# Performance work log

Hardware: AMD Instinct MI355X
Metric: run time of the kernel (lower is better)

The kernel has to match this reference:

```python
import jax, jax.numpy as jnp
import numpy as np
import math

B, L, D, H = 2, 1024, 1024, 16
DK = D // H  # 64
R = 130      # 2k+2 relative-position buckets (k=64)


def setup_inputs() -> dict:
    key = jax.random.key(0)
    ks = jax.random.split(key, 16)
    s = 1.0 / math.sqrt(D)
    return {
        "hidden_state": jax.random.normal(ks[0], (B, L, D), jnp.float32),
        "rel_q": jax.random.normal(ks[1], (1, H, R, DK), jnp.float32),
        "rel_k": jax.random.normal(ks[2], (1, H, R, DK), jnp.float32),
        "Wq": jax.random.normal(ks[3], (D, D), jnp.float32) * s,
        "bq": jnp.zeros((D,), jnp.float32),
        "Wk": jax.random.normal(ks[4], (D, D), jnp.float32) * s,
        "bk": jnp.zeros((D,), jnp.float32),
        "Wv": jax.random.normal(ks[5], (D, D), jnp.float32) * s,
        "bv": jnp.zeros((D,), jnp.float32),
        "Wo": jax.random.normal(ks[6], (D, D), jnp.float32) * s,
        "bo": jnp.zeros((D,), jnp.float32),
        "pos_indices": jax.random.randint(ks[7], (B, H, L, L), 0, R, jnp.int64 if jax.config.jax_enable_x64 else jnp.int32),
        "mask": jax.random.bernoulli(ks[8], 0.1, (B, 1, 1, L)),
    }


def reference(hidden_state, rel_q, rel_k, Wq, bq, Wk, bk, Wv, bv, Wo, bo, pos_indices, mask):
    # projections (torch Linear: x @ W.T + b), split into heads -> [B,H,L,DK]
    def proj(x, W, b):
        return (x @ W.T + b).reshape(B, L, H, DK).transpose(0, 2, 1, 3)

    q = proj(hidden_state, Wq, bq)
    k = proj(hidden_state, Wk, bk)
    v = proj(hidden_state, Wv, bv)

    scale = 1.0 / math.sqrt(DK * 3)  # scale_factor = 3 (c2c + p2c + c2p)

    # content-to-content: [B,H,L,L]
    c2c = jnp.einsum("bhid,bhjd->bhij", q, k) * scale

    # position-to-content: rel_q @ k.T -> [B,H,R,L], gather rows by pos_indices
    p2c = jnp.einsum("hrd,bhjd->bhrj", rel_q[0] * scale, k)
    p2c = jnp.take_along_axis(p2c, pos_indices, axis=-2)  # [B,H,L,L]

    # content-to-position: q @ rel_k.T -> [B,H,L,R], gather cols by pos_indices.T
    c2p = jnp.einsum("bhid,hrd->bhir", q, rel_k[0]) * scale
    c2p = jnp.take_along_axis(c2p, jnp.swapaxes(pos_indices, -2, -1), axis=-1)  # [B,H,L,L]

    scores = c2c + p2c + c2p
    scores = jnp.where(mask, jnp.float32(-1e9), scores)
    probs = jax.nn.softmax(scores, axis=-1)  # dropout p=0.0 (eval)

    ctx = jnp.einsum("bhij,bhjd->bhid", probs, v)
    out = ctx.transpose(0, 2, 1, 3).reshape(B, L, D) @ Wo.T + bo
    return out
```

## Files before the change

### kernel.cpp

```cpp
#include <hip/hip_runtime.h>
#include <hip/hip_fp16.h>

typedef _Float16 f16;
typedef f16 f16x8 __attribute__((ext_vector_type(8)));
typedef f16 f16x4 __attribute__((ext_vector_type(4)));
typedef float f32x4 __attribute__((ext_vector_type(4)));

#define DEVI static __device__ __forceinline__

constexpr int Bc = 2, Lc = 1024, Dc = 1024, Hc = 16, DKc = 64, Rc = 130;
constexpr float SCALE = 0.07216878364870323f;
constexpr float MASKV = -30000.0f;

DEVI uint2 pack8(int4 a, int4 b) {
    unsigned lo = (unsigned)(a.x & 255) | ((unsigned)(a.y & 255) << 8) |
                  ((unsigned)(a.z & 255) << 16) | ((unsigned)(a.w & 255) << 24);
    unsigned hi = (unsigned)(b.x & 255) | ((unsigned)(b.y & 255) << 8) |
                  ((unsigned)(b.z & 255) << 16) | ((unsigned)(b.w & 255) << 24);
    return make_uint2(lo, hi);
}

DEVI int i4get(const int4& v, int u) {
    return u == 0 ? v.x : (u == 1 ? v.y : (u == 2 ? v.z : v.w));
}

__global__ __launch_bounds__(256) void gemm_qkv(const float* __restrict__ A,
                                                const float* __restrict__ wq,
                                                const float* __restrict__ wk,
                                                const float* __restrict__ wv,
                                                const float* __restrict__ bq,
                                                const float* __restrict__ bk,
                                                const float* __restrict__ bv,
                                                f16* __restrict__ qw,
                                                f16* __restrict__ kw,
                                                f16* __restrict__ vtw) {
    constexpr int K = 1024;
    __shared__ __align__(16) f16 As[128][40];
    __shared__ __align__(16) f16 Bs[64][40];
    const int tid = threadIdx.x, lane = tid & 63, w = tid >> 6;
    const int wm = w >> 1, wn = w & 1;
    const int m0 = blockIdx.y * 128, n0 = blockIdx.x * 64;
    const int which = n0 >> 10;
    const float* __restrict__ W = which == 0 ? wq : (which == 1 ? wk : wv);
    const int n0L = n0 & 1023;

    f32x4 acc[4][2];
#pragma unroll
    for (int i = 0; i < 4; ++i)
#pragma unroll
        for (int j = 0; j < 2; ++j) acc[i][j] = (f32x4){0.f, 0.f, 0.f, 0.f};

    for (int k0 = 0; k0 < K; k0 += 32) {
#pragma unroll
        for (int rep = 0; rep < 4; ++rep) {
            int id = tid + rep * 256;
            int row = id >> 3, c = (id & 7) * 4;
            float4 v = *(const float4*)&A[(size_t)(m0 + row) * K + k0 + c];
            *(f16x4*)&As[row][c] = (f16x4){(f16)v.x, (f16)v.y, (f16)v.z, (f16)v.w};
        }
#pragma unroll
        for (int rep = 0; rep < 2; ++rep) {
            int id = tid + rep * 256;
            int row = id >> 3, c = (id & 7) * 4;
            float4 v = *(const float4*)&W[(size_t)(n0L + row) * K + k0 + c];
            *(f16x4*)&Bs[row][c] = (f16x4){(f16)v.x, (f16)v.y, (f16)v.z, (f16)v.w};
        }
        __syncthreads();
        f16x8 a[4], bb[2];
#pragma unroll
        for (int mf = 0; mf < 4; ++mf)
            a[mf] = *(const f16x8*)&As[wm * 64 + mf * 16 + (lane & 15)][(lane >> 4) * 8];
#pragma unroll
        for (int nf = 0; nf < 2; ++nf)
            bb[nf] = *(const f16x8*)&Bs[wn * 32 + nf * 16 + (lane & 15)][(lane >> 4) * 8];
#pragma unroll
        for (int mf = 0; mf < 4; ++mf)
#pragma unroll
            for (int nf = 0; nf < 2; ++nf)
                acc[mf][nf] = __builtin_amdgcn_mfma_f32_16x16x32_f16(a[mf], bb[nf], acc[mf][nf], 0, 0, 0);
        __syncthreads();
    }

    const float* bp = which == 0 ? bq : (which == 1 ? bk : bv);
    const float scl = which == 0 ? SCALE : 1.0f;
#pragma unroll
    for (int mf = 0; mf < 4; ++mf)
#pragma unroll
        for (int nf = 0; nf < 2; ++nf) {
            int rowb = m0 + wm * 64 + mf * 16 + (lane >> 4) * 4;
            int col = n0 + wn * 32 + nf * 16 + (lane & 15);
            int colL = col & 1023;
            int h = colL >> 6, d = colL & 63;
            float bv_ = bp[colL];
            if (which == 2) {
                int b = rowb >> 10, i = rowb & (Lc - 1);
                f16x4 pk = {(f16)(acc[mf][nf][0] + bv_), (f16)(acc[mf][nf][1] + bv_),
                            (f16)(acc[mf][nf][2] + bv_), (f16)(acc[mf][nf][3] + bv_)};
                *(f16x4*)&vtw[(((size_t)(b * Hc + h)) * DKc + d) * Lc + i] = pk;
            } else {
                f16* dst = which ? kw : qw;
#pragma unroll
                for (int rg = 0; rg < 4; ++rg) {
                    int row = rowb + rg;
                    int b = row >> 10, i = row & (Lc - 1);
                    dst[(((size_t)(b * Hc + h)) * Lc + i) * DKc + d] =
                        (f16)((acc[mf][nf][rg] + bv_) * scl);
                }
            }
        }
}

__global__ __launch_bounds__(256) void rel_mfma(const f16* __restrict__ rowmat,
                                                const float* __restrict__ relmat,
                                                f16* __restrict__ outT, float scl) {
    __shared__ __align__(16) f16 As[144][72];
    __shared__ __align__(16) f16 Bs[64][72];
    const int tid = threadIdx.x, lane = tid & 63, w = tid >> 6;
    const int bh = blockIdx.y, h = bh & (Hc - 1);
    const int i0 = blockIdx.x * 64;
    const size_t bhR = (size_t)bh * Rc;

    for (int e = tid; e < Rc * 16; e += 256) {
        int r = e >> 4, c = (e & 15) * 4;
        float4 v = *(const float4*)&relmat[((size_t)h * Rc + r) * DKc + c];
        *(f16x4*)&As[r][c] = (f16x4){(f16)v.x, (f16)v.y, (f16)v.z, (f16)v.w};
    }
    if (tid < 224) {
        int r = 130 + (tid >> 4), c = (tid & 15) * 4;
        *(f16x4*)&As[r][c] = (f16x4){(f16)0.f, (f16)0.f, (f16)0.f, (f16)0.f};
    }
    for (int e = tid; e < 64 * 8; e += 256) {
        int i = e >> 3, c = (e & 7) * 8;
        *(f16x8*)&Bs[i][c] = *(const f16x8*)&rowmat[((size_t)bh * Lc + i0 + i) * DKc + c];
    }
    __syncthreads();

    f16x8 bfr[2];
#pragma unroll
    for (int ks = 0; ks < 2; ++ks)
        bfr[ks] = *(const f16x8*)&Bs[w * 16 + (lane & 15)][ks * 32 + (lane >> 4) * 8];
    f32x4 acc[9];
#pragma unroll
    for (int m = 0; m < 9; ++m) acc[m] = (f32x4){0.f, 0.f, 0.f, 0.f};
#pragma unroll
    for (int m = 0; m < 9; ++m)
#pragma unroll
        for (int ks = 0; ks < 2; ++ks) {
            f16x8 af = *(const f16x8*)&As[m * 16 + (lane & 15)][ks * 32 + (lane >> 4) * 8];
            acc[m] = __builtin_amdgcn_mfma_f32_16x16x32_f16(af, bfr[ks], acc[m], 0, 0, 0);
        }
#pragma unroll
    for (int m = 0; m < 9; ++m)
#pragma unroll
        for (int rg = 0; rg < 4; ++rg) {
            int r = m * 16 + (lane >> 4) * 4 + rg;
            if (r < Rc)
                outT[(bhR + r) * Lc + i0 + w * 16 + (lane & 15)] = (f16)(acc[m][rg] * scl);
        }
}

__global__ __launch_bounds__(512) void attn_v8(const f16* __restrict__ q,
                                               const f16* __restrict__ k,
                                               const f16* __restrict__ vt,
                                               const f16* __restrict__ p2c,
                                               const f16* __restrict__ c2pT,
                                               const int* __restrict__ pos,
                                               const int* __restrict__ mask,
                                               f16* __restrict__ opart,
                                               float2* __restrict__ mlpart) {
    __shared__ f16 tc2p[Rc][132];
    __shared__ f16 tp2c[2][Rc][36];
    __shared__ __align__(16) f16 Ks[2][32][72];
    __shared__ unsigned char pJI[2][32][136];
    __shared__ float madd[2][32];
    __shared__ __align__(16) f16 Pl[8][16][32];

    const int tid = threadIdx.x, lane = tid & 63, w = tid >> 6;
    const int flat = blockIdx.x;
    const int ib = flat >> 6;
    const int sp = (flat >> 5) & 1;
    const int bh = flat & 31;
    const int b = bh >> 4, h = bh & 15;
    const int i0 = ib * 128;
    const int j0base = sp * 512;
    const size_t bhL = (size_t)bh * Lc;
    const size_t bhR = (size_t)bh * Rc;
    f16* __restrict__ op = opart + (size_t)sp * Bc * Lc * Dc;
    float2* __restrict__ mlp = mlpart + (size_t)sp * Bc * Hc * Lc;
    const int g = lane >> 4, il16 = lane & 15, irow = w * 16 + il16;

    for (int e = tid; e < Rc * 32; e += 512) {
        int r = e >> 5, c4 = (e & 31) * 4;
        *(f16x4*)&tc2p[r][c4] = *(const f16x4*)&c2pT[(bhR + r) * Lc + i0 + c4];
    }

    f16x8 qa[2];
    {
        const f16* qp = &q[(bhL + i0 + irow) * DKc + g * 8];
        qa[0] = *(const f16x8*)qp;
        qa[1] = *(const f16x8*)(qp + 32);
    }

    float mrun = -1e30f, lrun = 0.f;
    f32x4 oacc[4];
#pragma unroll
    for (int df = 0; df < 4; ++df) oacc[df] = (f32x4){0.f, 0.f, 0.f, 0.f};

    f16x4 kreg;
    int4 prA0, prA1, prB0, prB1;
    f16x4 tpr0, tpr1, tpr2;
    uint2 pjreg;
    float mreg;

#define FV_ISSUE(J0X)                                                                        \
    {                                                                                        \
        kreg = *(const f16x4*)&k[(bhL + (J0X) + (tid >> 4)) * DKc + (tid & 15) * 4];         \
        {                                                                                    \
            int e_ = tid;                                                                    \
            tpr0 = *(const f16x4*)&p2c[(bhR + (e_ >> 3)) * Lc + (J0X) + (e_ & 7) * 4];       \
            e_ = tid + 512;                                                                  \
            tpr1 = *(const f16x4*)&p2c[(bhR + (e_ >> 3)) * Lc + (J0X) + (e_ & 7) * 4];       \
            if (tid < 16) {                                                                  \
                e_ = tid + 1024;                                                             \
                tpr2 = *(const f16x4*)&p2c[(bhR + (e_ >> 3)) * Lc + (J0X) + (e_ & 7) * 4];   \
            }                                                                                \
        }                                                                                    \
        {                                                                                    \
            const int* pp = &pos[(bhL + (J0X) + (tid >> 4)) * Lc + i0 + (tid & 15) * 8];     \
            pjreg = pack8(*(const int4*)pp, *(const int4*)(pp + 4));                         \
        }                                                                                    \
        if (tid < 32) mreg = mask[b * Lc + (J0X) + tid] ? MASKV : 0.f;                       \
        {                                                                                    \
            const int* prow = &pos[(bhL + i0 + irow) * Lc + (J0X) + g * 4];                  \
            prB0 = *(const int4*)prow;                                                       \
            prB1 = *(const int4*)(prow + 16);                                                \
        }                                                                                    \
    }

#define FV_COMMIT(NB)                                                                        \
    {                                                                                        \
        *(f16x4*)&Ks[NB][tid >> 4][(tid & 15) * 4] = kreg;                                   \
        int e_ = tid;                                                                        \
        *(f16x4*)&tp2c[NB][e_ >> 3][(e_ & 7) * 4] = tpr0;                                    \
        e_ = tid + 512;                                                                      \
        *(f16x4*)&tp2c[NB][e_ >> 3][(e_ & 7) * 4] = tpr1;                                    \
        if (tid < 16) { e_ = tid + 1024; *(f16x4*)&tp2c[NB][e_ >> 3][(e_ & 7) * 4] = tpr2; } \
        *(uint2*)&pJI[NB][tid >> 4][(tid & 15) * 8] = pjreg;                                 \
        if (tid < 32) madd[NB][tid] = mreg;                                                  \
    }

    FV_ISSUE(j0base);
    FV_COMMIT(0);
    prA0 = prB0; prA1 = prB1;
    __syncthreads();

    for (int t = 0; t < 16; ++t) {
        const int cur = t & 1;
        const int j0 = j0base + t * 32;
        if (t < 15) FV_ISSUE(j0 + 32);

        f32x4 s[2];
        s[0] = (f32x4){0.f, 0.f, 0.f, 0.f};
        s[1] = (f32x4){0.f, 0.f, 0.f, 0.f};
#pragma unroll
        for (int jf = 0; jf < 2; ++jf)
#pragma unroll
            for (int ks = 0; ks < 2; ++ks) {
                f16x8 kb = *(const f16x8*)&Ks[cur][jf * 16 + il16][ks * 32 + g * 8];
                s[jf] = __builtin_amdgcn_mfma_f32_16x16x32_f16(kb, qa[ks], s[jf], 0, 0, 0);
            }

        f16x8 vf[4];
#pragma unroll
        for (int df = 0; df < 4; ++df)
            vf[df] = *(const f16x8*)&vt[((size_t)bh * DKc + df * 16 + il16) * Lc + j0 + g * 8];

        float sv[8];
#pragma unroll
        for (int u = 0; u < 8; ++u) {
            int jcol = (u < 4) ? (g * 4 + u) : (16 + g * 4 + (u - 4));
            int r1 = (u < 4) ? i4get(prA0, u) : i4get(prA1, u - 4);
            int r2 = pJI[cur][jcol][irow];
            sv[u] = s[u >> 2][u & 3] + (float)tp2c[cur][r1][jcol] +
                    (float)tc2p[r2][irow] + madd[cur][jcol];
        }

        float tm = sv[0];
#pragma unroll
        for (int e = 1; e < 8; ++e) tm = fmaxf(tm, sv[e]);
        tm = fmaxf(tm, __shfl_xor(tm, 16));
        tm = fmaxf(tm, __shfl_xor(tm, 32));
        float mnew = fmaxf(mrun, tm);
        float alpha = __expf(mrun - mnew);
        float rs = 0.f;
#pragma unroll
        for (int e = 0; e < 8; ++e) {
            sv[e] = __expf(sv[e] - mnew);
            rs += sv[e];
        }
        rs += __shfl_xor(rs, 16);
        rs += __shfl_xor(rs, 32);
        lrun = lrun * alpha + rs;
        mrun = mnew;

#pragma unroll
        for (int jf = 0; jf < 2; ++jf) {
            f16x4 pk = {(f16)sv[jf * 4 + 0], (f16)sv[jf * 4 + 1],
                        (f16)sv[jf * 4 + 2], (f16)sv[jf * 4 + 3]};
            *(f16x4*)&Pl[w][il16][jf * 16 + g * 4] = pk;
        }

        float al[4];
#pragma unroll
        for (int rg = 0; rg < 4; ++rg)
            al[rg] = __shfl(alpha, (lane & 48) | (g * 4 + rg));
#pragma unroll
        for (int df = 0; df < 4; ++df)
#pragma unroll
            for (int rg = 0; rg < 4; ++rg) oacc[df][rg] *= al[rg];

        f16x8 pa = *(const f16x8*)&Pl[w][il16][g * 8];
#pragma unroll
        for (int df = 0; df < 4; ++df)
            oacc[df] = __builtin_amdgcn_mfma_f32_16x16x32_f16(pa, vf[df], oacc[df], 0, 0, 0);

        if (t < 15) {
            FV_COMMIT(cur ^ 1);
            prA0 = prB0; prA1 = prB1;
        }
        __syncthreads();
    }

#pragma unroll
    for (int df = 0; df < 4; ++df)
#pragma unroll
        for (int rg = 0; rg < 4; ++rg) {
            int i = i0 + w * 16 + g * 4 + rg;
            int d = df * 16 + il16;
            op[((size_t)(b * Lc + i) * Hc + h) * DKc + d] = (f16)oacc[df][rg];
        }
    if (g == 0) mlp[bhL + i0 + irow] = make_float2(mrun, lrun);
#undef FV_ISSUE
#undef FV_COMMIT
}

__global__ __launch_bounds__(256) void merge_ns(const f16* __restrict__ op,
                                                const float2* __restrict__ ml,
                                                f16* __restrict__ ctx, int ns) {
    int t4 = blockIdx.x * 256 + threadIdx.x;
    int t = t4 * 4;
    int b = t >> 20;
    int rem = t & 1048575;
    int i = rem >> 10;
    int h = (rem & 1023) >> 6;
    int row = ((b << 4) + h) * Lc + i;
    const size_t On = (size_t)Bc * Lc * Dc, Mn = (size_t)Bc * Hc * Lc;
    float mx = -1e30f;
    for (int s = 0; s < ns; ++s) mx = fmaxf(mx, ml[s * Mn + row].x);
    float l = 0.f;
    float v[4] = {0.f, 0.f, 0.f, 0.f};
    for (int s = 0; s < ns; ++s) {
        float2 m = ml[s * Mn + row];
        float w_ = __expf(m.x - mx);
        l += m.y * w_;
        f16x4 o = *(const f16x4*)&op[s * On + t];
#pragma unroll
        for (int e = 0; e < 4; ++e) v[e] += (float)o[e] * w_;
    }
    float rl = 1.0f / l;
    f16x4 r = {(f16)(v[0] * rl), (f16)(v[1] * rl), (f16)(v[2] * rl), (f16)(v[3] * rl)};
    *(f16x4*)&ctx[t] = r;
}

__global__ __launch_bounds__(256) void gemm_out(const f16* __restrict__ A,
                                                const float* __restrict__ W,
                                                const float* __restrict__ bias,
                                                float* __restrict__ outf) {
    constexpr int K = 1024;
    __shared__ __align__(16) f16 As[128][40];
    __shared__ __align__(16) f16 Bs[64][40];
    const int tid = threadIdx.x, lane = tid & 63, w = tid >> 6;
    const int wm = w >> 1, wn = w & 1;
    const int m0 = blockIdx.y * 128, n0 = blockIdx.x * 64;

    f32x4 acc[4][2];
#pragma unroll
    for (int i = 0; i < 4; ++i)
#pragma unroll
        for (int j = 0; j < 2; ++j) acc[i][j] = (f32x4){0.f, 0.f, 0.f, 0.f};

    for (int k0 = 0; k0 < K; k0 += 32) {
#pragma unroll
        for (int rep = 0; rep < 2; ++rep) {
            int id = tid + rep * 256;
            int row = id >> 2, c = (id & 3) * 8;
            *(f16x8*)&As[row][c] = *(const f16x8*)&A[(size_t)(m0 + row) * K + k0 + c];
        }
#pragma unroll
        for (int rep = 0; rep < 2; ++rep) {
            int id = tid + rep * 256;
            int row = id >> 3, c = (id & 7) * 4;
            float4 v = *(const float4*)&W[(size_t)(n0 + row) * K + k0 + c];
            *(f16x4*)&Bs[row][c] = (f16x4){(f16)v.x, (f16)v.y, (f16)v.z, (f16)v.w};
        }
        __syncthreads();
        f16x8 a[4], bb[2];
#pragma unroll
        for (int mf = 0; mf < 4; ++mf)
            a[mf] = *(const f16x8*)&As[wm * 64 + mf * 16 + (lane & 15)][(lane >> 4) * 8];
#pragma unroll
        for (int nf = 0; nf < 2; ++nf)
            bb[nf] = *(const f16x8*)&Bs[wn * 32 + nf * 16 + (lane & 15)][(lane >> 4) * 8];
#pragma unroll
        for (int mf = 0; mf < 4; ++mf)
#pragma unroll
            for (int nf = 0; nf < 2; ++nf)
                acc[mf][nf] = __builtin_amdgcn_mfma_f32_16x16x32_f16(a[mf], bb[nf], acc[mf][nf], 0, 0, 0);
        __syncthreads();
    }
#pragma unroll
    for (int mf = 0; mf < 4; ++mf)
#pragma unroll
        for (int nf = 0; nf < 2; ++nf) {
            int rowb = m0 + wm * 64 + mf * 16 + (lane >> 4) * 4;
            int col = n0 + wn * 32 + nf * 16 + (lane & 15);
            float bv = bias[col];
#pragma unroll
            for (int rg = 0; rg < 4; ++rg)
                outf[(size_t)(rowb + rg) * Dc + col] = acc[mf][nf][rg] + bv;
        }
}

extern "C" void kernel_launch(void* const* d_in, const int* in_sizes, int n_in,
                              void* d_out, int out_size, void* d_ws, size_t ws_size,
                              hipStream_t stream) {
    const float* hid = (const float*)d_in[0];
    const float* rel_q = (const float*)d_in[1];
    const float* rel_k = (const float*)d_in[2];
    const float* Wq = (const float*)d_in[3];
    const float* bq = (const float*)d_in[4];
    const float* Wk = (const float*)d_in[5];
    const float* bk = (const float*)d_in[6];
    const float* Wv = (const float*)d_in[7];
    const float* bv = (const float*)d_in[8];
    const float* Wo = (const float*)d_in[9];
    const float* bo = (const float*)d_in[10];
    const int* pos = (const int*)d_in[11];
    const int* mask = (const int*)d_in[12];

    const size_t MiB = 1ull << 20;
    const size_t tblBytes = (size_t)Bc * Hc * Rc * Lc * 2;
    const size_t opBytes = (size_t)Bc * Lc * Dc * 2;
    const size_t mlBytes = (size_t)Bc * Hc * Lc * 8;
    const size_t need = (12 + 18 + 13) * MiB + 65536;
    if (need > ws_size) return;

    char* ws = (char*)d_ws;
    size_t off = 0;
    auto alloc = [&](size_t bytes) {
        void* p = ws + off;
        off += (bytes + 255) & ~(size_t)255;
        return p;
    };

    f16* qw = (f16*)alloc(opBytes);
    f16* kw = (f16*)alloc(opBytes);
    f16* vtw = (f16*)alloc(opBytes);
    f16* c2pTw = (f16*)alloc(tblBytes);
    f16* p2cw = (f16*)alloc(tblBytes);
    char* u = (char*)alloc(13 * MiB);
    f16* oparts = (f16*)u;
    float2* mls = (float2*)(u + 2 * opBytes);
    f16* ctxh = (f16*)(u + 2 * (opBytes + mlBytes));

    gemm_qkv<<<dim3(48, 16), 256, 0, stream>>>(hid, Wq, Wk, Wv, bq, bk, bv, qw, kw, vtw);
    rel_mfma<<<dim3(16, 32), 256, 0, stream>>>(qw, rel_k, c2pTw, 1.0f);
    rel_mfma<<<dim3(16, 32), 256, 0, stream>>>(kw, rel_q, p2cw, SCALE);
    attn_v8<<<512, 512, 0, stream>>>(qw, kw, vtw, p2cw, c2pTw, pos, mask, oparts, mls);
    merge_ns<<<2048, 256, 0, stream>>>(oparts, mls, ctxh, 2);
    gemm_out<<<dim3(16, 16), 256, 0, stream>>>(ctxh, Wo, bo, (float*)d_out);
}
```

Before: 150.1 us.

## Stage V tiles in shared memory and pass P via lane shuffles

The attention kernel now loads each V^T tile once per block into a double-buffered shared-memory buffer through the existing prefetch/commit pipeline, instead of every wave reading V directly from global memory inside the loop. The probability fragment for the PV MFMA is rebuilt with packed-f16 lane shuffles rather than a round trip through a per-wave shared-memory scratch buffer. This is meant to cut redundant global V traffic and LDS store/load latency in the inner loop. In exchange it adds LDS footprint for Vs and more shuffle instructions per iteration.

```diff
diff --git a/kernel.cpp b/kernel.cpp
--- a/kernel.cpp
+++ b/kernel.cpp
@@ -4,6 +4,7 @@
 typedef _Float16 f16;
 typedef f16 f16x8 __attribute__((ext_vector_type(8)));
 typedef f16 f16x4 __attribute__((ext_vector_type(4)));
+typedef f16 f16x2 __attribute__((ext_vector_type(2)));
 typedef float f32x4 __attribute__((ext_vector_type(4)));
 
 #define DEVI static __device__ __forceinline__
@@ -22,6 +23,11 @@
 
 DEVI int i4get(const int4& v, int u) {
     return u == 0 ? v.x : (u == 1 ? v.y : (u == 2 ? v.z : v.w));
+}
+
+DEVI int packf16(float a, float b) {
+    f16x2 t = {(f16)a, (f16)b};
+    return __builtin_bit_cast(int, t);
 }
 
 __global__ __launch_bounds__(256) void gemm_qkv(const float* __restrict__ A,
@@ -159,7 +165,7 @@
         }
 }
 
-__global__ __launch_bounds__(512) void attn_v8(const f16* __restrict__ q,
+__global__ __launch_bounds__(512) void attn_v9(const f16* __restrict__ q,
                                                const f16* __restrict__ k,
                                                const f16* __restrict__ vt,
                                                const f16* __restrict__ p2c,
@@ -171,9 +177,9 @@
     __shared__ f16 tc2p[Rc][132];
     __shared__ f16 tp2c[2][Rc][36];
     __shared__ __align__(16) f16 Ks[2][32][72];
+    __shared__ __align__(16) f16 Vs[2][64][40];
     __shared__ unsigned char pJI[2][32][136];
     __shared__ float madd[2][32];
-    __shared__ __align__(16) f16 Pl[8][16][32];
 
     const int tid = threadIdx.x, lane = tid & 63, w = tid >> 6;
     const int flat = blockIdx.x;
@@ -206,7 +212,7 @@
 #pragma unroll
     for (int df = 0; df < 4; ++df) oacc[df] = (f32x4){0.f, 0.f, 0.f, 0.f};
 
-    f16x4 kreg;
+    f16x4 kreg, vreg;
     int4 prA0, prA1, prB0, prB1;
     f16x4 tpr0, tpr1, tpr2;
     uint2 pjreg;
@@ -215,6 +221,7 @@
 #define FV_ISSUE(J0X)                                                                        \
     {                                                                                        \
         kreg = *(const f16x4*)&k[(bhL + (J0X) + (tid >> 4)) * DKc + (tid & 15) * 4];         \
+        vreg = *(const f16x4*)&vt[((size_t)bh * DKc + (tid >> 3)) * Lc + (J0X) + (tid & 7) * 4]; \
         {                                                                                    \
             int e_ = tid;                                                                    \
             tpr0 = *(const f16x4*)&p2c[(bhR + (e_ >> 3)) * Lc + (J0X) + (e_ & 7) * 4];       \
@@ -240,6 +247,7 @@
 #define FV_COMMIT(NB)                                                                        \
     {                                                                                        \
         *(f16x4*)&Ks[NB][tid >> 4][(tid & 15) * 4] = kreg;                                   \
+        *(f16x4*)&Vs[NB][tid >> 3][(tid & 7) * 4] = vreg;                                    \
         int e_ = tid;                                                                        \
         *(f16x4*)&tp2c[NB][e_ >> 3][(e_ & 7) * 4] = tpr0;                                    \
         e_ = tid + 512;                                                                      \
@@ -270,11 +278,6 @@
                 s[jf] = __builtin_amdgcn_mfma_f32_16x16x32_f16(kb, qa[ks], s[jf], 0, 0, 0);
             }
 
-        f16x8 vf[4];
-#pragma unroll
-        for (int df = 0; df < 4; ++df)
-            vf[df] = *(const f16x8*)&vt[((size_t)bh * DKc + df * 16 + il16) * Lc + j0 + g * 8];
-
         float sv[8];
 #pragma unroll
         for (int u = 0; u < 8; ++u) {
@@ -303,12 +306,15 @@
         lrun = lrun * alpha + rs;
         mrun = mnew;
 
-#pragma unroll
-        for (int jf = 0; jf < 2; ++jf) {
-            f16x4 pk = {(f16)sv[jf * 4 + 0], (f16)sv[jf * 4 + 1],
-                        (f16)sv[jf * 4 + 2], (f16)sv[jf * 4 + 3]};
-            *(f16x4*)&Pl[w][il16][jf * 16 + g * 4] = pk;
-        }
+        int lo0 = packf16(sv[0], sv[1]), lo1 = packf16(sv[2], sv[3]);
+        int hi0 = packf16(sv[4], sv[5]), hi1 = packf16(sv[6], sv[7]);
+        int s0 = ((g & 1) << 5) | il16, s1 = s0 + 16;
+        int a0 = __shfl(lo0, s0), a1 = __shfl(lo1, s0);
+        int a2 = __shfl(lo0, s1), a3 = __shfl(lo1, s1);
+        int b0 = __shfl(hi0, s0), b1 = __shfl(hi1, s0);
+        int b2 = __shfl(hi0, s1), b3 = __shfl(hi1, s1);
+        int4 paw = (g < 2) ? make_int4(a0, a1, a2, a3) : make_int4(b0, b1, b2, b3);
+        f16x8 pa = __builtin_bit_cast(f16x8, paw);
 
         float al[4];
 #pragma unroll
@@ -319,10 +325,11 @@
 #pragma unroll
             for (int rg = 0; rg < 4; ++rg) oacc[df][rg] *= al[rg];
 
-        f16x8 pa = *(const f16x8*)&Pl[w][il16][g * 8];
-#pragma unroll
-        for (int df = 0; df < 4; ++df)
-            oacc[df] = __builtin_amdgcn_mfma_f32_16x16x32_f16(pa, vf[df], oacc[df], 0, 0, 0);
+#pragma unroll
+        for (int df = 0; df < 4; ++df) {
+            f16x8 vb = *(const f16x8*)&Vs[cur][df * 16 + il16][g * 8];
+            oacc[df] = __builtin_amdgcn_mfma_f32_16x16x32_f16(pa, vb, oacc[df], 0, 0, 0);
+        }
 
         if (t < 15) {
             FV_COMMIT(cur ^ 1);
@@ -476,7 +483,7 @@
     gemm_qkv<<<dim3(48, 16), 256, 0, stream>>>(hid, Wq, Wk, Wv, bq, bk, bv, qw, kw, vtw);
     rel_mfma<<<dim3(16, 32), 256, 0, stream>>>(qw, rel_k, c2pTw, 1.0f);
     rel_mfma<<<dim3(16, 32), 256, 0, stream>>>(kw, rel_q, p2cw, SCALE);
-    attn_v8<<<512, 512, 0, stream>>>(qw, kw, vtw, p2cw, c2pTw, pos, mask, oparts, mls);
+    attn_v9<<<512, 512, 0, stream>>>(qw, kw, vtw, p2cw, c2pTw, pos, mask, oparts, mls);
     merge_ns<<<2048, 256, 0, stream>>>(oparts, mls, ctxh, 2);
     gemm_out<<<dim3(16, 16), 256, 0, stream>>>(ctxh, Wo, bo, (float*)d_out);
 }
```

Measured after the change: 131.2 us. 12.6% less time.
